# Performance work log

Measured on AMD Instinct MI355X. Metric: run time of the kernel, lower is better.

## Reference

```python
import jax, jax.numpy as jnp
import numpy as np

EPS = 1e-5  # torch nn.LayerNorm default


def layer_norm(x, g, b):
    mu = jnp.mean(x, axis=-1, keepdims=True)
    var = jnp.mean(jnp.square(x - mu), axis=-1, keepdims=True)
    return (x - mu) * jax.lax.rsqrt(var + EPS) * g + b


def run_dir(g_ih_seq, w_hh, g_hh, b_hh, g_ho, b_ho, reverse):
    """Run one LayerNormLSTMCell direction over precomputed LN(x @ W_ih^T).
    g_ih_seq: [S, B, 4H]. Returns final hidden [B, H]."""
    S, B, G = g_ih_seq.shape
    H = G // 4

    def step(carry, gih_t):
        h, c = carry
        gates = gih_t + layer_norm(h @ w_hh.T, g_hh, b_hh)  # [B, 4H]
        i, f, o = jnp.split(jax.nn.sigmoid(gates[:, : 3 * H]), 3, axis=1)
        g = jnp.tanh(gates[:, 3 * H :])
        c = f * c + i * g
        h = o * jnp.tanh(layer_norm(c, g_ho, b_ho))
        return (h, c), None

    z = jnp.zeros((B, H), g_ih_seq.dtype)
    (hT, _), _ = jax.lax.scan(step, (z, z), g_ih_seq, reverse=reverse)
    return hT


def lnlstm(x, w_ih0, w_hh0, ln_ih0_g, ln_ih0_b, ln_hh0_g, ln_hh0_b, ln_ho0_g,
           ln_ho0_b, w_ih1, w_hh1, ln_ih1_g, ln_ih1_b, ln_hh1_g, ln_hh1_b,
           ln_ho1_g, ln_ho1_b):
    # x: [B, S, E] -> permute(1,0,2)
    x_seq = jnp.transpose(x, (1, 0, 2))  # [S, B, E]
    S, B, _ = x_seq.shape

    # ---- layer 0 (time-varying input) ----
    g0f = layer_norm(jnp.einsum('sbe,ge->sbg', x_seq, w_ih0[0]), ln_ih0_g[0], ln_ih0_b[0])
    hf = run_dir(g0f, w_hh0[0], ln_hh0_g[0], ln_hh0_b[0], ln_ho0_g[0], ln_ho0_b[0], False)
    g0b = layer_norm(jnp.einsum('sbe,ge->sbg', x_seq, w_ih0[1]), ln_ih0_g[1], ln_ih0_b[1])
    hb = run_dir(g0b, w_hh0[1], ln_hh0_g[1], ln_hh0_b[1], ln_ho0_g[1], ln_ho0_b[1], True)

    # Due to the `[[None]*N]*seq_len` aliasing bug in the original torch code,
    # the next layer's input is the SAME vector at every timestep:
    xc = jnp.concatenate([hf, hb], axis=1)  # [B, 2H]

    # ---- layer 1 (constant input; LN(x@W_ih^T) computed once, broadcast over time) ----
    g1f = layer_norm(xc @ w_ih1[0].T, ln_ih1_g[0], ln_ih1_b[0])
    hf1 = run_dir(jnp.broadcast_to(g1f, (S,) + g1f.shape), w_hh1[0],
                  ln_hh1_g[0], ln_hh1_b[0], ln_ho1_g[0], ln_ho1_b[0], False)
    g1b = layer_norm(xc @ w_ih1[1].T, ln_ih1_g[1], ln_ih1_b[1])
    hb1 = run_dir(jnp.broadcast_to(g1b, (S,) + g1b.shape), w_hh1[1],
                  ln_hh1_g[1], ln_hh1_b[1], ln_ho1_g[1], ln_ho1_b[1], True)

    # y = max over time of identical vectors == the vector itself
    return jnp.concatenate([hf1, hb1], axis=1)  # [B, 2H]


def setup_inputs() -> dict:
    key = jax.random.key(0)
    ks = jax.random.split(key, 20)
    B, S, E, H = 64, 48, 512, 512
    f = jnp.float32
    n = jax.random.normal
    u = jax.random.uniform
    return {
        'x': n(ks[0], (B, S, E), f),
        'text_length': jax.random.randint(ks[1], (B,), 1, S),
        'w_ih0': n(ks[2], (2, 4 * H, E), f) * 0.05,
        'w_hh0': n(ks[3], (2, 4 * H, H), f) * 0.05,
        'ln_ih0_g': u(ks[4], (2, 4 * H), f, 0.5, 1.5),
        'ln_ih0_b': n(ks[5], (2, 4 * H), f) * 0.02,
        'ln_hh0_g': u(ks[6], (2, 4 * H), f, 0.5, 1.5),
        'ln_hh0_b': n(ks[7], (2, 4 * H), f) * 0.02,
        'ln_ho0_g': u(ks[8], (2, H), f, 0.5, 1.5),
        'ln_ho0_b': n(ks[9], (2, H), f) * 0.02,
        'w_ih1': n(ks[10], (2, 4 * H, 2 * H), f) * 0.05,
        'w_hh1': n(ks[11], (2, 4 * H, H), f) * 0.05,
        'ln_ih1_g': u(ks[12], (2, 4 * H), f, 0.5, 1.5),
        'ln_ih1_b': n(ks[13], (2, 4 * H), f) * 0.02,
        'ln_hh1_g': u(ks[14], (2, 4 * H), f, 0.5, 1.5),
        'ln_hh1_b': n(ks[15], (2, 4 * H), f) * 0.02,
        'ln_ho1_g': u(ks[16], (2, H), f, 0.5, 1.5),
        'ln_ho1_b': n(ks[17], (2, H), f) * 0.02,
    }


def reference(x, text_length, w_ih0, w_hh0, ln_ih0_g, ln_ih0_b, ln_hh0_g,
              ln_hh0_b, ln_ho0_g, ln_ho0_b, w_ih1, w_hh1, ln_ih1_g, ln_ih1_b,
              ln_hh1_g, ln_hh1_b, ln_ho1_g, ln_ho1_b):
    # text_length is accepted but unused by the original forward
    return lnlstm(x, w_ih0, w_hh0, ln_ih0_g, ln_ih0_b, ln_hh0_g, ln_hh0_b,
                  ln_ho0_g, ln_ho0_b, w_ih1, w_hh1, ln_ih1_g, ln_ih1_b,
                  ln_hh1_g, ln_hh1_b, ln_ho1_g, ln_ho1_b)
```

## Files before the change

### kernel.cpp

```cpp
#include <hip/hip_runtime.h>
#include <math.h>

#define HH 512
#define BB 64
#define SS 48
#define EE 512
#define G4 2048
#define EPSF 1e-5f
#define AGENT __HIP_MEMORY_SCOPE_AGENT

__device__ __forceinline__ float aload(const float* p) {
  return __hip_atomic_load(p, __ATOMIC_RELAXED, AGENT);
}
__device__ __forceinline__ void astore(float* p, float v) {
  __hip_atomic_store(p, v, __ATOMIC_RELAXED, AGENT);
}

__device__ __forceinline__ void gsync(int* c, int target) {
  __builtin_amdgcn_s_waitcnt(0);
  __syncthreads();
  if (threadIdx.x == 0) {
    __hip_atomic_fetch_add(c, 1, __ATOMIC_RELEASE, AGENT);
    int spins = 0;
    while (__hip_atomic_load(c, __ATOMIC_RELAXED, AGENT) < target) {
      __builtin_amdgcn_s_sleep(2);
      if (++spins > (1 << 21)) break;
    }
    (void)__hip_atomic_load(c, __ATOMIC_ACQUIRE, AGENT);
  }
  __syncthreads();
}

__global__ __launch_bounds__(256)
void gemm_ih0(const float* __restrict__ x, const float* __restrict__ w_ih0,
              float* __restrict__ G0) {
  __shared__ float As[16][65];
  __shared__ float Bs[16][65];
  const int m0 = blockIdx.y * 64;
  const int d  = m0 / (BB * SS);
  const float* Wm = w_ih0 + (size_t)d * G4 * EE;
  const int bn = blockIdx.x * 64;
  const int tid = threadIdx.x;
  const int lrow = tid >> 2;
  const int lkk  = (tid & 3) << 2;
  const int tx = tid & 15;
  const int ty = tid >> 4;
  int m  = m0 + lrow;
  int r  = m - d * (BB * SS);
  int b  = r / SS;
  int tl = r - b * SS;
  int s  = d ? (SS - 1 - tl) : tl;
  const float* arow = x + ((size_t)b * SS + s) * EE;

  float acc[4][4] = {};
  for (int k0 = 0; k0 < EE; k0 += 16) {
    float4 av = *(const float4*)(arow + k0 + lkk);
    float4 bv = *(const float4*)(Wm + (size_t)(bn + lrow) * EE + k0 + lkk);
    As[lkk+0][lrow] = av.x; As[lkk+1][lrow] = av.y; As[lkk+2][lrow] = av.z; As[lkk+3][lrow] = av.w;
    Bs[lkk+0][lrow] = bv.x; Bs[lkk+1][lrow] = bv.y; Bs[lkk+2][lrow] = bv.z; Bs[lkk+3][lrow] = bv.w;
    __syncthreads();
    #pragma unroll
    for (int k = 0; k < 16; ++k) {
      float a[4], bbv[4];
      #pragma unroll
      for (int i = 0; i < 4; ++i) a[i] = As[k][ty*4+i];
      #pragma unroll
      for (int j = 0; j < 4; ++j) bbv[j] = Bs[k][tx*4+j];
      #pragma unroll
      for (int i = 0; i < 4; ++i)
        #pragma unroll
        for (int j = 0; j < 4; ++j) acc[i][j] += a[i]*bbv[j];
    }
    __syncthreads();
  }
  for (int i = 0; i < 4; ++i)
    for (int j = 0; j < 4; ++j)
      G0[(size_t)(m0 + ty*4 + i) * G4 + bn + tx*4 + j] = acc[i][j];
}

__global__ __launch_bounds__(256)
void ln_rows(float* __restrict__ X, const float* __restrict__ gamma,
             const float* __restrict__ beta, int rows_per_d) {
  __shared__ float red[8];
  const int row = blockIdx.x;
  const int d = row / rows_per_d;
  float* xr = X + (size_t)row * G4;
  const float* gg = gamma + (size_t)d * G4;
  const float* bb = beta  + (size_t)d * G4;
  float s = 0.f, q = 0.f;
  float v[8];
  #pragma unroll
  for (int it = 0; it < 8; ++it) {
    float xv = xr[threadIdx.x + it*256];
    v[it] = xv; s += xv; q += xv*xv;
  }
  #pragma unroll
  for (int off = 32; off > 0; off >>= 1) { s += __shfl_down(s, off); q += __shfl_down(q, off); }
  int lane = threadIdx.x & 63, wid = threadIdx.x >> 6;
  if (lane == 0) { red[wid] = s; red[4+wid] = q; }
  __syncthreads();
  float ts = red[0]+red[1]+red[2]+red[3];
  float tq = red[4]+red[5]+red[6]+red[7];
  float mu = ts * (1.f/G4);
  float rstd = rsqrtf(tq*(1.f/G4) - mu*mu + EPSF);
  #pragma unroll
  for (int it = 0; it < 8; ++it) {
    int jc = threadIdx.x + it*256;
    xr[jc] = (v[it]-mu)*rstd*gg[jc] + bb[jc];
  }
}

__global__ __launch_bounds__(1024, 4)
void persist7(const float* __restrict__ whh, const float* __restrict__ Gbuf,
              long g_row_stride, long g_t_stride,
              const float* __restrict__ lnhg, const float* __restrict__ lnhb,
              const float* __restrict__ lnog, const float* __restrict__ lnob,
              float* cbuf, float* obuf, float* Rpart, float* Cpart,
              int* flagsA, int* flagsB,
              float* fout, int nsteps,
              int mode1, const float* __restrict__ w_ih1,
              const float* __restrict__ xcb, float* g1pre,
              const float* __restrict__ ln_g1, const float* __restrict__ ln_b1,
              int* cnt_pre) {
  __shared__ float hlds[16][1024];
  __shared__ float part[16][8][64];
  __shared__ float redR[16][64];
  __shared__ float bcR[16][2];
  __shared__ float bcC[16][2];
  __shared__ float sred[32];

  const int bb = blockIdx.x;
  const int tid = threadIdx.x;

  if (mode1) {
    const int dp = bb & 1, nbp = bb >> 1;
    const int pb = tid >> 4, ns = tid & 15;
    const int col = nbp*16 + ns;
    const float* xrow = xcb + (size_t)pb * 1024;
    const float* wv_ = w_ih1 + ((size_t)dp*G4 + col) * 1024;
    float a = 0.f;
    for (int k = 0; k < 1024; k += 4) {
      float4 xv = *(const float4*)(xrow + k);
      float4 wv4 = *(const float4*)(wv_ + k);
      a += xv.x*wv4.x + xv.y*wv4.y + xv.z*wv4.z + xv.w*wv4.w;
    }
    astore(g1pre + ((size_t)dp*BB + pb) * G4 + col, a);
    gsync(cnt_pre + 0, 256);
    if (bb < 128) {
      const int ld = bb >> 6;
      float* xr = g1pre + (size_t)bb * G4;
      const float* gg = ln_g1 + (size_t)ld * G4;
      const float* be = ln_b1 + (size_t)ld * G4;
      float v0 = aload(xr + tid), v1 = aload(xr + tid + 1024);
      float s = v0 + v1, q = v0*v0 + v1*v1;
      #pragma unroll
      for (int off = 32; off > 0; off >>= 1) { s += __shfl_down(s, off); q += __shfl_down(q, off); }
      const int wv2 = tid >> 6;
      if ((tid & 63) == 0) { sred[wv2] = s; sred[16+wv2] = q; }
      __syncthreads();
      float ts = 0.f, tq = 0.f;
      #pragma unroll
      for (int i = 0; i < 16; ++i) { ts += sred[i]; tq += sred[16+i]; }
      float mu = ts * (1.f/G4);
      float rstd = rsqrtf(tq*(1.f/G4) - mu*mu + EPSF);
      astore(xr + tid,        (v0-mu)*rstd*gg[tid]      + be[tid]);
      astore(xr + tid + 1024, (v1-mu)*rstd*gg[tid+1024] + be[tid+1024]);
    }
    gsync(cnt_pre + 16, 256);
  }

  const int g  = bb & 7;
  const int d  = g >> 2;
  const int bq = g & 3;
  const int jb = bb >> 3;
  const int rowbase = d*BB + bq*16;
  const int ke = tid >> 6, nl = tid & 63;
  const int ncol = jb*16 + ((nl>>4) << 9) + (nl & 15);
  int* fA = flagsA + g*1024;
  int* fB = flagsB + g*1024;

  float wreg[32];
  {
    const float* wp = whh + ((size_t)d*G4 + ncol)*HH + (size_t)ke*32;
    #pragma unroll
    for (int i = 0; i < 32; ++i) wreg[i] = wp[i];
  }

  const int bl = tid >> 4, jl = tid & 15;
  const int rowc = rowbase + bl;
  const int jc = jb*16 + jl;
  const int scol = tid & 511, srh = tid >> 9;
  const float ogv = lnog[(size_t)d*HH + scol];
  const float obv = lnob[(size_t)d*HH + scol];
  const int row16 = tid >> 5, j32 = tid & 31;
  const int inv_g = (g_t_stride == 0);

  float hg0=0,hg1=0,hg2=0,hg3=0, hb0=0,hb1=0,hb2=0,hb3=0;
  float cg0=0,cg1=0,cg2=0,cg3=0;
  if (tid < 256) {
    const float* lnhg_d = lnhg + (size_t)d*G4;
    const float* lnhb_d = lnhb + (size_t)d*G4;
    hg0 = lnhg_d[jc];        hb0 = lnhb_d[jc];
    hg1 = lnhg_d[HH+jc];     hb1 = lnhb_d[HH+jc];
    hg2 = lnhg_d[2*HH+jc];   hb2 = lnhb_d[2*HH+jc];
    hg3 = lnhg_d[3*HH+jc];   hb3 = lnhb_d[3*HH+jc];
    if (inv_g) {
      const float* gr = Gbuf + (size_t)rowc * g_row_stride;
      cg0 = gr[jc]; cg1 = gr[HH+jc]; cg2 = gr[2*HH+jc]; cg3 = gr[3*HH+jc];
    }
  }
  float creg = 0.f;

  for (int t = 0; t < nsteps; ++t) {
    float cv[8], ovv[8];
    #pragma unroll
    for (int i = 0; i < 8; ++i) {
      int row = i*2 + srh;
      cv[i]  = aload(cbuf + (size_t)(rowbase + row)*512 + scol);
      ovv[i] = aload(obuf + (size_t)(rowbase + row)*512 + scol);
    }
    if (tid < 512) {
      float s = aload(Cpart + ((size_t)(rowbase+row16)*32 + j32)*2 + 0);
      float q = aload(Cpart + ((size_t)(rowbase+row16)*32 + j32)*2 + 1);
      #pragma unroll
      for (int off = 16; off > 0; off >>= 1) { s += __shfl_down(s, off, 32); q += __shfl_down(q, off, 32); }
      if (j32 == 0) {
        float mu = s * (1.f/HH);
        bcC[row16][0] = mu;
        bcC[row16][1] = rsqrtf(q*(1.f/HH) - mu*mu + EPSF);
      }
    }
    __syncthreads();
    #pragma unroll
    for (int i = 0; i < 8; ++i) {
      int row = i*2 + srh;
      hlds[row][scol] = ovv[i] * tanhf((cv[i] - bcC[row][0]) * bcC[row][1] * ogv + obv);
    }
    __syncthreads();

    #pragma unroll
    for (int half = 0; half < 2; ++half) {
      #pragma unroll
      for (int b = 0; b < 8; ++b) {
        const float* hp = &hlds[half*8 + b][ke*32];
        float acc = 0.f;
        #pragma unroll
        for (int i4 = 0; i4 < 8; ++i4) {
          float4 h4 = *(const float4*)(hp + 4*i4);
          acc += h4.x*wreg[4*i4+0] + h4.y*wreg[4*i4+1]
               + h4.z*wreg[4*i4+2] + h4.w*wreg[4*i4+3];
        }
        part[ke][b][nl] = acc;
      }
      __syncthreads();
      if (tid < 512) {
        int b = tid >> 6, n2 = tid & 63;
        float r = 0.f;
        #pragma unroll
        for (int k16 = 0; k16 < 16; ++k16) r += part[k16][b][n2];
        redR[half*8 + b][n2] = r;
      }
      __syncthreads();
    }
    if (tid < 512) {
      float v1 = redR[row16][j32], v2 = redR[row16][j32+32];
      float s = v1 + v2, q = v1*v1 + v2*v2;
      #pragma unroll
      for (int off = 16; off > 0; off >>= 1) { s += __shfl_down(s, off, 32); q += __shfl_down(q, off, 32); }
      if (j32 == 0) {
        astore(Rpart + ((size_t)(rowbase+row16)*32 + jb)*2 + 0, s);
        astore(Rpart + ((size_t)(rowbase+row16)*32 + jb)*2 + 1, q);
      }
    }
    float pg0 = cg0, pg1 = cg1, pg2 = cg2, pg3 = cg3;
    if (tid < 256 && !inv_g) {
      const float* gr = Gbuf + (size_t)rowc * g_row_stride + (size_t)t * g_t_stride;
      pg0 = gr[jc]; pg1 = gr[HH+jc]; pg2 = gr[2*HH+jc]; pg3 = gr[3*HH+jc];
    }
    __syncthreads();
    if (tid == 0) __hip_atomic_store(fA + jb*32, t + 1, __ATOMIC_RELAXED, AGENT);
    if (tid < 32) {
      int spins = 0;
      for (;;) {
        int v = __hip_atomic_load(fA + tid*32, __ATOMIC_RELAXED, AGENT);
        #pragma unroll
        for (int off = 16; off > 0; off >>= 1) v = min(v, __shfl_down(v, off, 32));
        v = __shfl(v, 0, 32);
        if (v >= t + 1) break;
        __builtin_amdgcn_s_sleep(1);
        if (++spins > (1 << 22)) break;
      }
    }
    __syncthreads();

    if (tid < 512) {
      float s = aload(Rpart + ((size_t)(rowbase+row16)*32 + j32)*2 + 0);
      float q = aload(Rpart + ((size_t)(rowbase+row16)*32 + j32)*2 + 1);
      #pragma unroll
      for (int off = 16; off > 0; off >>= 1) { s += __shfl_down(s, off, 32); q += __shfl_down(q, off, 32); }
      if (j32 == 0) {
        float mu = s * (1.f/G4);
        bcR[row16][0] = mu;
        bcR[row16][1] = rsqrtf(q*(1.f/G4) - mu*mu + EPSF);
      }
    }
    __syncthreads();

    if (tid < 256) {
      float mu = bcR[bl][0], rstd = bcR[bl][1];
      float gi = pg0 + (redR[bl][jl]    - mu)*rstd*hg0 + hb0;
      float gf = pg1 + (redR[bl][16+jl] - mu)*rstd*hg1 + hb1;
      float go = pg2 + (redR[bl][32+jl] - mu)*rstd*hg2 + hb2;
      float gt = pg3 + (redR[bl][48+jl] - mu)*rstd*hg3 + hb3;
      float iv = 1.f/(1.f+expf(-gi)), fv = 1.f/(1.f+expf(-gf));
      float ov = 1.f/(1.f+expf(-go)), gv = tanhf(gt);
      creg = fv*creg + iv*gv;
      float cs = creg, cq = creg*creg;
      #pragma unroll
      for (int off = 8; off > 0; off >>= 1) { cs += __shfl_down(cs, off, 16); cq += __shfl_down(cq, off, 16); }
      if (jl == 0) {
        astore(Cpart + ((size_t)rowc*32 + jb)*2 + 0, cs);
        astore(Cpart + ((size_t)rowc*32 + jb)*2 + 1, cq);
      }
      astore(cbuf + (size_t)rowc*512 + jc, creg);
      astore(obuf + (size_t)rowc*512 + jc, ov);
    }
    __syncthreads();
    if (tid == 0) __hip_atomic_store(fB + jb*32, t + 1, __ATOMIC_RELAXED, AGENT);
    if (tid < 32) {
      int spins = 0;
      for (;;) {
        int v = __hip_atomic_load(fB + tid*32, __ATOMIC_RELAXED, AGENT);
        #pragma unroll
        for (int off = 16; off > 0; off >>= 1) v = min(v, __shfl_down(v, off, 32));
        v = __shfl(v, 0, 32);
        if (v >= t + 1) break;
        __builtin_amdgcn_s_sleep(1);
        if (++spins > (1 << 22)) break;
      }
    }
    __syncthreads();
  }

  {
    float cv[8], ovv[8];
    #pragma unroll
    for (int i = 0; i < 8; ++i) {
      int row = i*2 + srh;
      cv[i]  = aload(cbuf + (size_t)(rowbase + row)*512 + scol);
      ovv[i] = aload(obuf + (size_t)(rowbase + row)*512 + scol);
    }
    if (tid < 512) {
      float s = aload(Cpart + ((size_t)(rowbase+row16)*32 + j32)*2 + 0);
      float q = aload(Cpart + ((size_t)(rowbase+row16)*32 + j32)*2 + 1);
      #pragma unroll
      for (int off = 16; off > 0; off >>= 1) { s += __shfl_down(s, off, 32); q += __shfl_down(q, off, 32); }
      if (j32 == 0) {
        float mu = s * (1.f/HH);
        bcC[row16][0] = mu;
        bcC[row16][1] = rsqrtf(q*(1.f/HH) - mu*mu + EPSF);
      }
    }
    __syncthreads();
    if (jb == 0) {
      #pragma unroll
      for (int i = 0; i < 8; ++i) {
        int row = i*2 + srh;
        float h = ovv[i] * tanhf((cv[i] - bcC[row][0]) * bcC[row][1] * ogv + obv);
        fout[(size_t)(bq*16 + row) * 1024 + (size_t)d*512 + scol] = h;
      }
    }
  }
}

extern "C" void kernel_launch(void* const* d_in, const int* in_sizes, int n_in,
                              void* d_out, int out_size, void* d_ws, size_t ws_size,
                              hipStream_t stream) {
  const float* x        = (const float*)d_in[0];
  const float* w_ih0    = (const float*)d_in[2];
  const float* w_hh0    = (const float*)d_in[3];
  const float* ln_ih0_g = (const float*)d_in[4];
  const float* ln_ih0_b = (const float*)d_in[5];
  const float* ln_hh0_g = (const float*)d_in[6];
  const float* ln_hh0_b = (const float*)d_in[7];
  const float* ln_ho0_g = (const float*)d_in[8];
  const float* ln_ho0_b = (const float*)d_in[9];
  const float* w_ih1    = (const float*)d_in[10];
  const float* w_hh1    = (const float*)d_in[11];
  const float* ln_ih1_g = (const float*)d_in[12];
  const float* ln_ih1_b = (const float*)d_in[13];
  const float* ln_hh1_g = (const float*)d_in[14];
  const float* ln_hh1_b = (const float*)d_in[15];
  const float* ln_ho1_g = (const float*)d_in[16];
  const float* ln_ho1_b = (const float*)d_in[17];
  float* out = (float*)d_out;

  float* G0    = (float*)d_ws;
  float* g1pre = G0 + (size_t)2*BB*SS*G4;
  float* xcb   = g1pre + (size_t)2*BB*G4;
  float* Rpart = xcb + (size_t)BB*1024;
  float* Cpart = Rpart + (size_t)128*32*2;
  float* cbuf  = Cpart + (size_t)128*32*2;
  float* obuf  = cbuf + (size_t)128*512;
  int*   ints  = (int*)(obuf + (size_t)128*512);
  int*   fA0     = ints;
  int*   fB0     = ints + 8192;
  int*   fA1     = ints + 16384;
  int*   fB1     = ints + 24576;
  int*   cnt_pre = ints + 32768;

  hipMemsetAsync(Cpart, 0, ((size_t)128*32*2 + 2*(size_t)128*512)*sizeof(float)
                           + 32832*sizeof(int), stream);

  hipLaunchKernelGGL(gemm_ih0, dim3(G4/64, (2*BB*SS)/64), dim3(256), 0, stream,
      x, w_ih0, G0);
  hipLaunchKernelGGL(ln_rows, dim3(2*BB*SS), dim3(256), 0, stream,
      G0, ln_ih0_g, ln_ih0_b, BB*SS);

  hipLaunchKernelGGL(persist7, dim3(256), dim3(1024), 0, stream,
      w_hh0, G0, (long)SS*G4, (long)G4,
      ln_hh0_g, ln_hh0_b, ln_ho0_g, ln_ho0_b,
      cbuf, obuf, Rpart, Cpart, fA0, fB0, xcb, SS,
      0, (const float*)nullptr, (const float*)nullptr, (float*)nullptr,
      (const float*)nullptr, (const float*)nullptr, (int*)nullptr);

  hipMemsetAsync(Cpart, 0, ((size_t)128*32*2 + 2*(size_t)128*512)*sizeof(float), stream);

  hipLaunchKernelGGL(persist7, dim3(256), dim3(1024), 0, stream,
      w_hh1, g1pre, (long)G4, 0L,
      ln_hh1_g, ln_hh1_b, ln_ho1_g, ln_ho1_b,
      cbuf, obuf, Rpart, Cpart, fA1, fB1, out, SS,
      1, w_ih1, xcb, g1pre, ln_ih1_g, ln_ih1_b, cnt_pre);
}
```

Before: 1.847 ms.

## Replace per-step grid barriers with per-wave flag polling and pack state as float2

Each wave now polls the cross-block flags itself instead of thread 0 spinning and the block doing a __syncthreads. That removes two block-wide barriers and the shared-memory broadcasts of LayerNorm statistics on every timestep. The c and o state are packed into one float2 buffer, and the partial sum/sumsq pairs are packed too, so each exchange is a single 64-bit atomic load or store. Row statistics are reduced with wave shuffles, and expf/tanhf are replaced with clamped __expf-based sigmoid and tanh. The fast math slightly changes numerics, and many waves polling raises traffic on the flag lines.

```diff
diff --git a/kernel.cpp b/kernel.cpp
--- a/kernel.cpp
+++ b/kernel.cpp
@@ -8,12 +8,42 @@
 #define G4 2048
 #define EPSF 1e-5f
 #define AGENT __HIP_MEMORY_SCOPE_AGENT
+typedef unsigned long long ull;
 
 __device__ __forceinline__ float aload(const float* p) {
   return __hip_atomic_load(p, __ATOMIC_RELAXED, AGENT);
 }
 __device__ __forceinline__ void astore(float* p, float v) {
   __hip_atomic_store(p, v, __ATOMIC_RELAXED, AGENT);
+}
+__device__ __forceinline__ float2 aloadf2(const float2* p) {
+  ull u = __hip_atomic_load((const ull*)p, __ATOMIC_RELAXED, AGENT);
+  union { ull u; float2 f; } x; x.u = u; return x.f;
+}
+__device__ __forceinline__ void astoref2(float2* p, float2 v) {
+  union { ull u; float2 f; } x; x.f = v;
+  __hip_atomic_store((ull*)p, x.u, __ATOMIC_RELAXED, AGENT);
+}
+
+__device__ __forceinline__ float fsig(float x) {
+  x = fminf(fmaxf(x, -30.f), 30.f);
+  return 1.f / (1.f + __expf(-x));
+}
+__device__ __forceinline__ float ftanh(float x) {
+  float e = __expf(fminf(fmaxf(2.f*x, -60.f), 60.f));
+  return (e - 1.f) / (e + 1.f);
+}
+
+__device__ __forceinline__ void wdetect(const int* f, int target) {
+  int spins = 0;
+  for (;;) {
+    int v = __hip_atomic_load(f + (threadIdx.x & 31)*32, __ATOMIC_RELAXED, AGENT);
+    #pragma unroll
+    for (int off = 16; off > 0; off >>= 1) v = min(v, __shfl_xor(v, off, 32));
+    if (v >= target) break;
+    __builtin_amdgcn_s_sleep(1);
+    if (++spins > (1 << 22)) break;
+  }
 }
 
 __device__ __forceinline__ void gsync(int* c, int target) {
@@ -111,11 +141,11 @@
 }
 
 __global__ __launch_bounds__(1024, 4)
-void persist7(const float* __restrict__ whh, const float* __restrict__ Gbuf,
+void persist8(const float* __restrict__ whh, const float* __restrict__ Gbuf,
               long g_row_stride, long g_t_stride,
               const float* __restrict__ lnhg, const float* __restrict__ lnhb,
               const float* __restrict__ lnog, const float* __restrict__ lnob,
-              float* cbuf, float* obuf, float* Rpart, float* Cpart,
+              float2* cobuf, float2* Rpart, float2* Cpart,
               int* flagsA, int* flagsB,
               float* fout, int nsteps,
               int mode1, const float* __restrict__ w_ih1,
@@ -125,12 +155,11 @@
   __shared__ float hlds[16][1024];
   __shared__ float part[16][8][64];
   __shared__ float redR[16][64];
-  __shared__ float bcR[16][2];
-  __shared__ float bcC[16][2];
   __shared__ float sred[32];
 
   const int bb = blockIdx.x;
   const int tid = threadIdx.x;
+  const int l = tid & 63;
 
   if (mode1) {
     const int dp = bb & 1, nbp = bb >> 1;
@@ -156,7 +185,7 @@
       #pragma unroll
       for (int off = 32; off > 0; off >>= 1) { s += __shfl_down(s, off); q += __shfl_down(q, off); }
       const int wv2 = tid >> 6;
-      if ((tid & 63) == 0) { sred[wv2] = s; sred[16+wv2] = q; }
+      if (l == 0) { sred[wv2] = s; sred[16+wv2] = q; }
       __syncthreads();
       float ts = 0.f, tq = 0.f;
       #pragma unroll
@@ -174,8 +203,8 @@
   const int bq = g & 3;
   const int jb = bb >> 3;
   const int rowbase = d*BB + bq*16;
-  const int ke = tid >> 6, nl = tid & 63;
-  const int ncol = jb*16 + ((nl>>4) << 9) + (nl & 15);
+  const int ke = tid >> 6;
+  const int ncol = jb*16 + ((l>>4) << 9) + (l & 15);
   int* fA = flagsA + g*1024;
   int* fB = flagsB + g*1024;
 
@@ -194,6 +223,8 @@
   const float obv = lnob[(size_t)d*HH + scol];
   const int row16 = tid >> 5, j32 = tid & 31;
   const int inv_g = (g_t_stride == 0);
+  const int strow = rowbase + ((l >> 3) << 1) + srh;
+  const int stslot = (l & 7) * 4;
 
   float hg0=0,hg1=0,hg2=0,hg3=0, hb0=0,hb1=0,hb2=0,hb3=0;
   float cg0=0,cg1=0,cg2=0,cg3=0;
@@ -212,29 +243,28 @@
   float creg = 0.f;
 
   for (int t = 0; t < nsteps; ++t) {
-    float cv[8], ovv[8];
-    #pragma unroll
-    for (int i = 0; i < 8; ++i) {
-      int row = i*2 + srh;
-      cv[i]  = aload(cbuf + (size_t)(rowbase + row)*512 + scol);
-      ovv[i] = aload(obuf + (size_t)(rowbase + row)*512 + scol);
-    }
-    if (tid < 512) {
-      float s = aload(Cpart + ((size_t)(rowbase+row16)*32 + j32)*2 + 0);
-      float q = aload(Cpart + ((size_t)(rowbase+row16)*32 + j32)*2 + 1);
-      #pragma unroll
-      for (int off = 16; off > 0; off >>= 1) { s += __shfl_down(s, off, 32); q += __shfl_down(q, off, 32); }
-      if (j32 == 0) {
-        float mu = s * (1.f/HH);
-        bcC[row16][0] = mu;
-        bcC[row16][1] = rsqrtf(q*(1.f/HH) - mu*mu + EPSF);
+    wdetect(fB, t);
+    {
+      float2 co[8];
+      #pragma unroll
+      for (int i = 0; i < 8; ++i)
+        co[i] = aloadf2(cobuf + (size_t)(rowbase + i*2 + srh)*512 + scol);
+      float s = 0.f, q = 0.f;
+      #pragma unroll
+      for (int m = 0; m < 4; ++m) {
+        float2 p = aloadf2(Cpart + (size_t)strow*32 + stslot + m);
+        s += p.x; q += p.y;
       }
-    }
-    __syncthreads();
-    #pragma unroll
-    for (int i = 0; i < 8; ++i) {
-      int row = i*2 + srh;
-      hlds[row][scol] = ovv[i] * tanhf((cv[i] - bcC[row][0]) * bcC[row][1] * ogv + obv);
+      #pragma unroll
+      for (int off = 4; off > 0; off >>= 1) { s += __shfl_xor(s, off, 8); q += __shfl_xor(q, off, 8); }
+      #pragma unroll
+      for (int i = 0; i < 8; ++i) {
+        float si = __shfl(s, i*8, 64);
+        float qi = __shfl(q, i*8, 64);
+        float mu = si * (1.f/HH);
+        float rs = rsqrtf(qi*(1.f/HH) - mu*mu + EPSF);
+        hlds[i*2 + srh][scol] = co[i].y * ftanh((co[i].x - mu)*rs*ogv + obv);
+      }
     }
     __syncthreads();
 
@@ -250,7 +280,7 @@
           acc += h4.x*wreg[4*i4+0] + h4.y*wreg[4*i4+1]
                + h4.z*wreg[4*i4+2] + h4.w*wreg[4*i4+3];
         }
-        part[ke][b][nl] = acc;
+        part[ke][b][l] = acc;
       }
       __syncthreads();
       if (tid < 512) {
@@ -267,10 +297,8 @@
       float s = v1 + v2, q = v1*v1 + v2*v2;
       #pragma unroll
       for (int off = 16; off > 0; off >>= 1) { s += __shfl_down(s, off, 32); q += __shfl_down(q, off, 32); }
-      if (j32 == 0) {
-        astore(Rpart + ((size_t)(rowbase+row16)*32 + jb)*2 + 0, s);
-        astore(Rpart + ((size_t)(rowbase+row16)*32 + jb)*2 + 1, q);
-      }
+      if (j32 == 0)
+        astoref2(Rpart + (size_t)(rowbase+row16)*32 + jb, make_float2(s, q));
     }
     float pg0 = cg0, pg1 = cg1, pg2 = cg2, pg3 = cg3;
     if (tid < 256 && !inv_g) {
@@ -279,96 +307,56 @@
     }
     __syncthreads();
     if (tid == 0) __hip_atomic_store(fA + jb*32, t + 1, __ATOMIC_RELAXED, AGENT);
-    if (tid < 32) {
-      int spins = 0;
-      for (;;) {
-        int v = __hip_atomic_load(fA + tid*32, __ATOMIC_RELAXED, AGENT);
-        #pragma unroll
-        for (int off = 16; off > 0; off >>= 1) v = min(v, __shfl_down(v, off, 32));
-        v = __shfl(v, 0, 32);
-        if (v >= t + 1) break;
-        __builtin_amdgcn_s_sleep(1);
-        if (++spins > (1 << 22)) break;
-      }
-    }
-    __syncthreads();
-
-    if (tid < 512) {
-      float s = aload(Rpart + ((size_t)(rowbase+row16)*32 + j32)*2 + 0);
-      float q = aload(Rpart + ((size_t)(rowbase+row16)*32 + j32)*2 + 1);
-      #pragma unroll
-      for (int off = 16; off > 0; off >>= 1) { s += __shfl_down(s, off, 32); q += __shfl_down(q, off, 32); }
-      if (j32 == 0) {
-        float mu = s * (1.f/G4);
-        bcR[row16][0] = mu;
-        bcR[row16][1] = rsqrtf(q*(1.f/G4) - mu*mu + EPSF);
-      }
-    }
-    __syncthreads();
 
     if (tid < 256) {
-      float mu = bcR[bl][0], rstd = bcR[bl][1];
+      wdetect(fA, t + 1);
+      float2 pa = aloadf2(Rpart + (size_t)rowc*32 + jl);
+      float2 pb = aloadf2(Rpart + (size_t)rowc*32 + jl + 16);
+      float s2 = pa.x + pb.x, q2 = pa.y + pb.y;
+      #pragma unroll
+      for (int off = 8; off > 0; off >>= 1) { s2 += __shfl_xor(s2, off, 16); q2 += __shfl_xor(q2, off, 16); }
+      float mu = s2 * (1.f/G4);
+      float rstd = rsqrtf(q2*(1.f/G4) - mu*mu + EPSF);
       float gi = pg0 + (redR[bl][jl]    - mu)*rstd*hg0 + hb0;
       float gf = pg1 + (redR[bl][16+jl] - mu)*rstd*hg1 + hb1;
       float go = pg2 + (redR[bl][32+jl] - mu)*rstd*hg2 + hb2;
       float gt = pg3 + (redR[bl][48+jl] - mu)*rstd*hg3 + hb3;
-      float iv = 1.f/(1.f+expf(-gi)), fv = 1.f/(1.f+expf(-gf));
-      float ov = 1.f/(1.f+expf(-go)), gv = tanhf(gt);
+      float iv = fsig(gi), fv = fsig(gf), ov = fsig(go), gv = ftanh(gt);
       creg = fv*creg + iv*gv;
       float cs = creg, cq = creg*creg;
       #pragma unroll
-      for (int off = 8; off > 0; off >>= 1) { cs += __shfl_down(cs, off, 16); cq += __shfl_down(cq, off, 16); }
-      if (jl == 0) {
-        astore(Cpart + ((size_t)rowc*32 + jb)*2 + 0, cs);
-        astore(Cpart + ((size_t)rowc*32 + jb)*2 + 1, cq);
-      }
-      astore(cbuf + (size_t)rowc*512 + jc, creg);
-      astore(obuf + (size_t)rowc*512 + jc, ov);
+      for (int off = 8; off > 0; off >>= 1) { cs += __shfl_xor(cs, off, 16); cq += __shfl_xor(cq, off, 16); }
+      if (jl == 0)
+        astoref2(Cpart + (size_t)rowc*32 + jb, make_float2(cs, cq));
+      astoref2(cobuf + (size_t)rowc*512 + jc, make_float2(creg, ov));
     }
     __syncthreads();
     if (tid == 0) __hip_atomic_store(fB + jb*32, t + 1, __ATOMIC_RELAXED, AGENT);
-    if (tid < 32) {
-      int spins = 0;
-      for (;;) {
-        int v = __hip_atomic_load(fB + tid*32, __ATOMIC_RELAXED, AGENT);
-        #pragma unroll
-        for (int off = 16; off > 0; off >>= 1) v = min(v, __shfl_down(v, off, 32));
-        v = __shfl(v, 0, 32);
-        if (v >= t + 1) break;
-        __builtin_amdgcn_s_sleep(1);
-        if (++spins > (1 << 22)) break;
-      }
-    }
-    __syncthreads();
-  }
-
-  {
-    float cv[8], ovv[8];
+  }
+
+  if (jb == 0) {
+    wdetect(fB, nsteps);
+    float2 co[8];
+    #pragma unroll
+    for (int i = 0; i < 8; ++i)
+      co[i] = aloadf2(cobuf + (size_t)(rowbase + i*2 + srh)*512 + scol);
+    float s = 0.f, q = 0.f;
+    #pragma unroll
+    for (int m = 0; m < 4; ++m) {
+      float2 p = aloadf2(Cpart + (size_t)strow*32 + stslot + m);
+      s += p.x; q += p.y;
+    }
+    #pragma unroll
+    for (int off = 4; off > 0; off >>= 1) { s += __shfl_xor(s, off, 8); q += __shfl_xor(q, off, 8); }
     #pragma unroll
     for (int i = 0; i < 8; ++i) {
+      float si = __shfl(s, i*8, 64);
+      float qi = __shfl(q, i*8, 64);
+      float mu = si * (1.f/HH);
+      float rs = rsqrtf(qi*(1.f/HH) - mu*mu + EPSF);
       int row = i*2 + srh;
-      cv[i]  = aload(cbuf + (size_t)(rowbase + row)*512 + scol);
-      ovv[i] = aload(obuf + (size_t)(rowbase + row)*512 + scol);
-    }
-    if (tid < 512) {
-      float s = aload(Cpart + ((size_t)(rowbase+row16)*32 + j32)*2 + 0);
-      float q = aload(Cpart + ((size_t)(rowbase+row16)*32 + j32)*2 + 1);
-      #pragma unroll
-      for (int off = 16; off > 0; off >>= 1) { s += __shfl_down(s, off, 32); q += __shfl_down(q, off, 32); }
-      if (j32 == 0) {
-        float mu = s * (1.f/HH);
-        bcC[row16][0] = mu;
-        bcC[row16][1] = rsqrtf(q*(1.f/HH) - mu*mu + EPSF);
-      }
-    }
-    __syncthreads();
-    if (jb == 0) {
-      #pragma unroll
-      for (int i = 0; i < 8; ++i) {
-        int row = i*2 + srh;
-        float h = ovv[i] * tanhf((cv[i] - bcC[row][0]) * bcC[row][1] * ogv + obv);
-        fout[(size_t)(bq*16 + row) * 1024 + (size_t)d*512 + scol] = h;
-      }
+      float h = co[i].y * ftanh((co[i].x - mu)*rs*ogv + obv);
+      fout[(size_t)(bq*16 + row) * 1024 + (size_t)d*512 + scol] = h;
     }
   }
 }
@@ -395,21 +383,20 @@
   const float* ln_ho1_b = (const float*)d_in[17];
   float* out = (float*)d_out;
 
-  float* G0    = (float*)d_ws;
-  float* g1pre = G0 + (size_t)2*BB*SS*G4;
-  float* xcb   = g1pre + (size_t)2*BB*G4;
-  float* Rpart = xcb + (size_t)BB*1024;
-  float* Cpart = Rpart + (size_t)128*32*2;
-  float* cbuf  = Cpart + (size_t)128*32*2;
-  float* obuf  = cbuf + (size_t)128*512;
-  int*   ints  = (int*)(obuf + (size_t)128*512);
-  int*   fA0     = ints;
-  int*   fB0     = ints + 8192;
-  int*   fA1     = ints + 16384;
-  int*   fB1     = ints + 24576;
-  int*   cnt_pre = ints + 32768;
-
-  hipMemsetAsync(Cpart, 0, ((size_t)128*32*2 + 2*(size_t)128*512)*sizeof(float)
+  float*  G0    = (float*)d_ws;
+  float*  g1pre = G0 + (size_t)2*BB*SS*G4;
+  float*  xcb   = g1pre + (size_t)2*BB*G4;
+  float2* Rpart = (float2*)(xcb + (size_t)BB*1024);
+  float2* Cpart = Rpart + (size_t)128*32;
+  float2* cobuf = Cpart + (size_t)128*32;
+  int*    ints  = (int*)(cobuf + (size_t)128*512);
+  int*    fA0     = ints;
+  int*    fB0     = ints + 8192;
+  int*    fA1     = ints + 16384;
+  int*    fB1     = ints + 24576;
+  int*    cnt_pre = ints + 32768;
+
+  hipMemsetAsync(Cpart, 0, ((size_t)128*32 + (size_t)128*512)*sizeof(float2)
                            + 32832*sizeof(int), stream);
 
   hipLaunchKernelGGL(gemm_ih0, dim3(G4/64, (2*BB*SS)/64), dim3(256), 0, stream,
@@ -417,18 +404,18 @@
   hipLaunchKernelGGL(ln_rows, dim3(2*BB*SS), dim3(256), 0, stream,
       G0, ln_ih0_g, ln_ih0_b, BB*SS);
 
-  hipLaunchKernelGGL(persist7, dim3(256), dim3(1024), 0, stream,
+  hipLaunchKernelGGL(persist8, dim3(256), dim3(1024), 0, stream,
       w_hh0, G0, (long)SS*G4, (long)G4,
       ln_hh0_g, ln_hh0_b, ln_ho0_g, ln_ho0_b,
-      cbuf, obuf, Rpart, Cpart, fA0, fB0, xcb, SS,
+      cobuf, Rpart, Cpart, fA0, fB0, xcb, SS,
       0, (const float*)nullptr, (const float*)nullptr, (float*)nullptr,
       (const float*)nullptr, (const float*)nullptr, (int*)nullptr);
 
-  hipMemsetAsync(Cpart, 0, ((size_t)128*32*2 + 2*(size_t)128*512)*sizeof(float), stream);
-
-  hipLaunchKernelGGL(persist7, dim3(256), dim3(1024), 0, stream,
+  hipMemsetAsync(Cpart, 0, ((size_t)128*32 + (size_t)128*512)*sizeof(float2), stream);
+
+  hipLaunchKernelGGL(persist8, dim3(256), dim3(1024), 0, stream,
       w_hh1, g1pre, (long)G4, 0L,
       ln_hh1_g, ln_hh1_b, ln_ho1_g, ln_ho1_b,
-      cbuf, obuf, Rpart, Cpart, fA1, fB1, out, SS,
+      cobuf, Rpart, Cpart, fA1, fB1, out, SS,
       1, w_ih1, xcb, g1pre, ln_ih1_g, ln_ih1_b, cnt_pre);
 }
```

Result: slower. 1.896 ms (+2.6%).
